# Performance work log

Measured on AMD Instinct MI355X. Metric: run time of the kernel, lower is better.

## Reference

```python
import jax, jax.numpy as jnp
import numpy as np

NBODY = 63          # body 0 = world, body 1 = free-joint root, bodies 2..62 = hinge
NHINGE = NBODY - 2  # 61 hinge dofs -> qpos dim = 7 + 61 = 68
NSITES = 16
B = 131072


def _qmul(q1, q2):
    """Hamilton product, (w,x,y,z) convention. Broadcasts over leading dims."""
    w1, x1, y1, z1 = q1[..., 0], q1[..., 1], q1[..., 2], q1[..., 3]
    w2, x2, y2, z2 = q2[..., 0], q2[..., 1], q2[..., 2], q2[..., 3]
    return jnp.stack([
        w1 * w2 - x1 * x2 - y1 * y2 - z1 * z2,
        w1 * x2 + x1 * w2 + y1 * z2 - z1 * y2,
        w1 * y2 - x1 * z2 + y1 * w2 + z1 * x2,
        w1 * z2 + x1 * y2 - y1 * x2 + z1 * w2,
    ], axis=-1)


def _qrot(q, v):
    """Rotate v by unit quaternion q (equivalent to q*v*q^-1 sandwich)."""
    u = q[..., 1:]
    w = q[..., :1]
    t = 2.0 * jnp.cross(u, v)
    return v + w * t + jnp.cross(u, t)


def setup_inputs() -> dict:
    key = jax.random.key(0)
    ks = jax.random.split(key, 8)
    qpos = jax.random.normal(ks[0], (B, 7 + NHINGE), dtype=jnp.float32) * 0.3
    body_pos = jax.random.normal(ks[1], (NBODY, 3), dtype=jnp.float32) * 0.1
    bq = jax.random.normal(ks[2], (NBODY, 4), dtype=jnp.float32)
    body_quat = bq / jnp.linalg.norm(bq, axis=-1, keepdims=True)
    ax = jax.random.normal(ks[3], (NHINGE, 3), dtype=jnp.float32)
    hinge_axis = ax / jnp.linalg.norm(ax, axis=-1, keepdims=True)
    jnt_pos = jax.random.normal(ks[4], (NHINGE, 3), dtype=jnp.float32) * 0.05
    site_pos = jax.random.normal(ks[5], (NSITES, 3), dtype=jnp.float32) * 0.05
    body_parent = jnp.maximum(jnp.arange(NBODY, dtype=jnp.int32) - 1, 0)  # chain tree
    site_body = jax.random.randint(ks[6], (NSITES,), 1, NBODY, dtype=jnp.int32)
    return {
        'qpos': qpos, 'body_pos': body_pos, 'body_quat': body_quat,
        'hinge_axis': hinge_axis, 'jnt_pos': jnt_pos, 'site_pos': site_pos,
        'body_parent': body_parent, 'site_body': site_body,
    }


def reference(qpos, body_pos, body_quat, hinge_axis, jnt_pos, site_pos,
              body_parent, site_body):
    # Structural ints are static tree topology: pull to host for Python indexing.
    parents = np.asarray(body_parent)
    sbody = np.asarray(site_body)
    Bn = qpos.shape[0]
    nbody = body_pos.shape[0]

    wp = [None] * nbody  # per-body world position [B,3]
    wq = [None] * nbody  # per-body world quaternion [B,4]
    wp[0] = jnp.zeros((Bn, 3), dtype=qpos.dtype)
    wq[0] = jnp.broadcast_to(jnp.array([1.0, 0.0, 0.0, 0.0], dtype=qpos.dtype), (Bn, 4))

    # body 1: free joint -> root pos + normalized quat straight from qpos
    wp[1] = qpos[:, 0:3]
    q = qpos[:, 3:7]
    wq[1] = q / jnp.linalg.norm(q, axis=-1, keepdims=True)

    # hinge bodies, parents always processed before children
    for bid in range(2, nbody):
        h = bid - 2
        p = int(parents[bid])
        half = 0.5 * qpos[:, 7 + h]
        s, c = jnp.sin(half), jnp.cos(half)
        ax = hinge_axis[h]
        hq = jnp.stack([c, s * ax[0], s * ax[1], s * ax[2]], axis=-1)  # [B,4]
        local_combined = _qmul(jnp.broadcast_to(body_quat[bid], (Bn, 4)), hq)
        anchor = wp[p] + _qrot(wq[p], body_pos[bid] + jnt_pos[h])  # world joint anchor
        nq = _qmul(wq[p], local_combined)
        wq[bid] = nq
        wp[bid] = anchor - _qrot(nq, jnt_pos[h])

    WP = jnp.stack(wp, axis=1)  # [B, nbody, 3]
    WQ = jnp.stack(wq, axis=1)  # [B, nbody, 4]

    # sites: vectorized gather + rotate over all keypoint sites at once
    sq = WQ[:, sbody]                         # [B, S, 4]
    sp = WP[:, sbody]                         # [B, S, 3]
    sites = sp + _qrot(sq, site_pos[None, :, :])  # [B, S, 3]
    return sites
```

## Files before the change

### kernel.cpp

```cpp
#include <hip/hip_runtime.h>


#define NBODY  63
#define NHINGE 61
#define NSITES 16
#define QDIM   68
#define LSTRIDE 49
#define INV2PI 0.15915494309189535f

typedef unsigned int u32;

#define HC_OFF   0
#define SP_OFF   (NHINGE * 16)
#define MASK_OFF (SP_OFF + NSITES * 4)
#define BM_OFF   (MASK_OFF + 64)

__global__ void fk_setup(const float* __restrict__ body_pos, const float* __restrict__ body_quat,
                         const float* __restrict__ hinge_axis, const float* __restrict__ jnt_pos,
                         const float* __restrict__ site_pos, const int* __restrict__ site_body,
                         float* __restrict__ ws)
{
    int tid = threadIdx.x;
    if (tid < NHINGE) {
        int h = tid, bid = h + 2;
        float uw = body_quat[bid*4+0], ux = body_quat[bid*4+1];
        float uy = body_quat[bid*4+2], uz = body_quat[bid*4+3];
        float ax = hinge_axis[h*3+0], ay = hinge_axis[h*3+1], az = hinge_axis[h*3+2];
        float jx = jnt_pos[h*3+0],   jy = jnt_pos[h*3+1],   jz = jnt_pos[h*3+2];
        float bx = body_pos[bid*3+0], by = body_pos[bid*3+1], bz = body_pos[bid*3+2];
        float* o = ws + HC_OFF + h * 16;
        o[0] = uw; o[1] = ux; o[2] = uy; o[3] = uz;
        o[4] = -(ux * ax + uy * ay + uz * az);
        o[5] =  uw * ax + uy * az - uz * ay;
        o[6] =  uw * ay - ux * az + uz * ax;
        o[7] =  uw * az + ux * ay - uy * ax;
        o[8] = bx + jx; o[9] = by + jy; o[10] = bz + jz; o[11] = 0.f;
        o[12] = jx; o[13] = jy; o[14] = jz; o[15] = 0.f;
    }
    if (tid < NSITES) {
        float* o = ws + SP_OFF + tid * 4;
        o[0] = site_pos[tid*3+0];
        o[1] = site_pos[tid*3+1];
        o[2] = site_pos[tid*3+2];
        o[3] = 0.f;
    }
    if (tid == 0) {
        int* im = (int*)(ws + MASK_OFF);
        unsigned long long bm = 0ull;
        for (int b = 0; b < NBODY; b++) {
            int m = 0;
            for (int s = 0; s < NSITES; s++)
                if (site_body[s] == b) m |= (1 << s);
            im[b] = m;
            if (m) bm |= (1ull << b);
        }
        u32* pbm = (u32*)(ws + BM_OFF);
        pbm[0] = (u32)bm; pbm[1] = (u32)(bm >> 32);
    }
}

__global__ __launch_bounds__(256, 2)
void fk_main(const float* __restrict__ qpos, const float* __restrict__ ws,
             float* __restrict__ out)
{
    __shared__ float sbuf[256 * LSTRIDE];
    const int tid = threadIdx.x;
    const int t = blockIdx.x * 256 + tid;
    float* my = sbuf + tid * LSTRIDE;

    float f[QDIM];
    const float4* q4 = reinterpret_cast<const float4*>(qpos) + (size_t)t * 17;
#pragma unroll
    for (int i = 0; i < 17; i++) {
        float4 v = q4[i];
        f[4*i+0] = v.x; f[4*i+1] = v.y; f[4*i+2] = v.z; f[4*i+3] = v.w;
    }

    const u32* pbm = (const u32*)(ws + BM_OFF);
    unsigned long long bodymask = ((unsigned long long)pbm[1] << 32) | (unsigned long long)pbm[0];
    const int* im = (const int*)(ws + MASK_OFF);

    float wpx = f[0], wpy = f[1], wpz = f[2];
    float qw = f[3], qx = f[4], qy = f[5], qz = f[6];
    float inv = rsqrtf(qw * qw + qx * qx + qy * qy + qz * qz);
    qw *= inv; qx *= inv; qy *= inv; qz *= inv;

    auto emit = [&](int bid) {
        int m = im[bid];
        while (m) {
            int s = __ffs(m) - 1; m &= m - 1;
            const float* sp = ws + SP_OFF + s * 4;
            float vx = sp[0], vy = sp[1], vz = sp[2];
            float tx = 2.f * (qy * vz - qz * vy);
            float ty = 2.f * (qz * vx - qx * vz);
            float tz = 2.f * (qx * vy - qy * vx);
            float* o = my + s * 3;
            o[0] = wpx + vx + qw * tx + (qy * tz - qz * ty);
            o[1] = wpy + vy + qw * ty + (qz * tx - qx * tz);
            o[2] = wpz + vz + qw * tz + (qx * ty - qy * tx);
        }
    };

    if (bodymask & 2ull) emit(1);

#pragma unroll
    for (int h = 0; h < NHINGE; h++) {
        const int bid = h + 2;
        const float* c = ws + HC_OFF + h * 16;
        float rev = (0.5f * INV2PI) * f[7 + h];
        float sn = __builtin_amdgcn_sinf(rev);
        float cs = __builtin_amdgcn_cosf(rev);
        float lw = cs * c[0] + sn * c[4];
        float lx = cs * c[1] + sn * c[5];
        float ly = cs * c[2] + sn * c[6];
        float lz = cs * c[3] + sn * c[7];
        float ax = c[8], ay = c[9], az = c[10];
        float tx = 2.f * (qy * az - qz * ay);
        float ty = 2.f * (qz * ax - qx * az);
        float tz = 2.f * (qx * ay - qy * ax);
        float anx = wpx + ax + qw * tx + (qy * tz - qz * ty);
        float any_ = wpy + ay + qw * ty + (qz * tx - qx * tz);
        float anz = wpz + az + qw * tz + (qx * ty - qy * tx);
        float nw = qw * lw - qx * lx - qy * ly - qz * lz;
        float nx = qw * lx + qx * lw + qy * lz - qz * ly;
        float ny = qw * ly - qx * lz + qy * lw + qz * lx;
        float nz = qw * lz + qx * ly - qy * lx + qz * lw;
        float jx = c[12], jy = c[13], jz = c[14];
        float t2x = 2.f * (ny * jz - nz * jy);
        float t2y = 2.f * (nz * jx - nx * jz);
        float t2z = 2.f * (nx * jy - ny * jx);
        wpx = anx - (jx + nw * t2x + (ny * t2z - nz * t2y));
        wpy = any_ - (jy + nw * t2y + (nz * t2x - nx * t2z));
        wpz = anz - (jz + nw * t2z + (nx * t2y - ny * t2x));
        qw = nw; qx = nx; qy = ny; qz = nz;

        if (bodymask & (1ull << bid)) emit(bid);
    }

    __syncthreads();

    {
        size_t blk_dw = (size_t)blockIdx.x * (256 * 48);
        float4* out4 = reinterpret_cast<float4*>(out + blk_dw);
#pragma unroll
        for (int k = 0; k < 12; k++) {
            int g = k * 256 + tid;
            int q = g / 12;
            int r = (g - q * 12) * 4;
            const float* p = sbuf + q * LSTRIDE + r;
            float4 v = { p[0], p[1], p[2], p[3] };
            out4[g] = v;
        }
    }
}

extern "C" void kernel_launch(void* const* d_in, const int* in_sizes, int n_in,
                              void* d_out, int out_size, void* d_ws, size_t ws_size,
                              hipStream_t stream)
{
    const float* qpos       = (const float*)d_in[0];
    const float* body_pos   = (const float*)d_in[1];
    const float* body_quat  = (const float*)d_in[2];
    const float* hinge_axis = (const float*)d_in[3];
    const float* jnt_pos    = (const float*)d_in[4];
    const float* site_pos   = (const float*)d_in[5];
    const int* site_body    = (const int*)d_in[7];
    float* ws = (float*)d_ws;

    int nb = in_sizes[0] / QDIM;

    fk_setup<<<1, 64, 0, stream>>>(body_pos, body_quat, hinge_axis, jnt_pos,
                                   site_pos, site_body, ws);
    fk_main<<<nb / 256, 256, 0, stream>>>(qpos, ws, (float*)d_out);
}
```

Before: 133.0 us.

## Transpose qpos to column-major in a pre-pass and stream hinge angles via window

Adds a separate kernel that transposes qpos into a column-major scratch buffer so the main kernel can do coalesced per-column loads. The main kernel then keeps a small rotating window of hinge angles in registers instead of holding all 68 floats, which lowers register pressure and allows more blocks per CU. The cost is an extra full read and write of qpos through global memory plus one more kernel launch.

```diff
diff --git a/kernel.cpp b/kernel.cpp
--- a/kernel.cpp
+++ b/kernel.cpp
@@ -7,6 +7,7 @@
 #define QDIM   68
 #define LSTRIDE 49
 #define INV2PI 0.15915494309189535f
+#define WIN 8
 
 typedef unsigned int u32;
 
@@ -14,6 +15,7 @@
 #define SP_OFF   (NHINGE * 16)
 #define MASK_OFF (SP_OFF + NSITES * 4)
 #define BM_OFF   (MASK_OFF + 64)
+#define QT_OFF   4096
 
 __global__ void fk_setup(const float* __restrict__ body_pos, const float* __restrict__ body_quat,
                          const float* __restrict__ hinge_axis, const float* __restrict__ jnt_pos,
@@ -59,29 +61,54 @@
     }
 }
 
-__global__ __launch_bounds__(256, 2)
-void fk_main(const float* __restrict__ qpos, const float* __restrict__ ws,
-             float* __restrict__ out)
+__global__ __launch_bounds__(256, 4)
+void fk_transpose(const float* __restrict__ qpos, float* __restrict__ qT, int nb)
+{
+    __shared__ float tile[64][QDIM + 1];
+    const int k = threadIdx.x;
+    const int rowbase = blockIdx.x * 64;
+    const float* src = qpos + (size_t)rowbase * QDIM;
+#pragma unroll
+    for (int i = 0; i < 17; i++) {
+        int g = i * 256 + k;
+        tile[g / QDIM][g % QDIM] = src[g];
+    }
+    __syncthreads();
+    const int sub = k & 63;
+    const int grp = k >> 6;
+#pragma unroll
+    for (int i = 0; i < 17; i++) {
+        int e = grp + 4 * i;
+        qT[(size_t)e * nb + rowbase + sub] = tile[sub][e];
+    }
+}
+
+__global__ __launch_bounds__(256, 3)
+void fk_main(const float* __restrict__ ws, float* __restrict__ out, int nb)
 {
     __shared__ float sbuf[256 * LSTRIDE];
     const int tid = threadIdx.x;
     const int t = blockIdx.x * 256 + tid;
     float* my = sbuf + tid * LSTRIDE;
 
-    float f[QDIM];
-    const float4* q4 = reinterpret_cast<const float4*>(qpos) + (size_t)t * 17;
-#pragma unroll
-    for (int i = 0; i < 17; i++) {
-        float4 v = q4[i];
-        f[4*i+0] = v.x; f[4*i+1] = v.y; f[4*i+2] = v.z; f[4*i+3] = v.w;
-    }
+    const float* qT = ws + QT_OFF;
 
     const u32* pbm = (const u32*)(ws + BM_OFF);
     unsigned long long bodymask = ((unsigned long long)pbm[1] << 32) | (unsigned long long)pbm[0];
     const int* im = (const int*)(ws + MASK_OFF);
 
-    float wpx = f[0], wpy = f[1], wpz = f[2];
-    float qw = f[3], qx = f[4], qy = f[5], qz = f[6];
+    float wpx = qT[(size_t)0 * nb + t];
+    float wpy = qT[(size_t)1 * nb + t];
+    float wpz = qT[(size_t)2 * nb + t];
+    float qw  = qT[(size_t)3 * nb + t];
+    float qx  = qT[(size_t)4 * nb + t];
+    float qy  = qT[(size_t)5 * nb + t];
+    float qz  = qT[(size_t)6 * nb + t];
+
+    float win[WIN];
+#pragma unroll
+    for (int i = 0; i < WIN; i++) win[i] = qT[(size_t)(7 + i) * nb + t];
+
     float inv = rsqrtf(qw * qw + qx * qx + qy * qy + qz * qz);
     qw *= inv; qx *= inv; qy *= inv; qz *= inv;
 
@@ -107,7 +134,10 @@
     for (int h = 0; h < NHINGE; h++) {
         const int bid = h + 2;
         const float* c = ws + HC_OFF + h * 16;
-        float rev = (0.5f * INV2PI) * f[7 + h];
+        float ang = win[h & (WIN - 1)];
+        if (h + WIN < NHINGE)
+            win[h & (WIN - 1)] = qT[(size_t)(7 + h + WIN) * nb + t];
+        float rev = (0.5f * INV2PI) * ang;
         float sn = __builtin_amdgcn_sinf(rev);
         float cs = __builtin_amdgcn_cosf(rev);
         float lw = cs * c[0] + sn * c[4];
@@ -171,5 +201,6 @@
 
     fk_setup<<<1, 64, 0, stream>>>(body_pos, body_quat, hinge_axis, jnt_pos,
                                    site_pos, site_body, ws);
-    fk_main<<<nb / 256, 256, 0, stream>>>(qpos, ws, (float*)d_out);
-}
+    fk_transpose<<<nb / 64, 256, 0, stream>>>(qpos, ws + QT_OFF, nb);
+    fk_main<<<nb / 256, 256, 0, stream>>>(ws, (float*)d_out, nb);
+}
```

Result: slower. 145.7 us (+9.5%).
